# Optimization experiments

Measured on AMD Instinct MI355X. Metric: run time of the kernel, lower is better.

## Reference

```python
import jax, jax.numpy as jnp
import numpy as np
from jax import lax

D_MODEL = 512
INPUT_DIM = 64
D_INNER = 1024      # expand * d_model
D_STATE = 128
NHEADS = 16         # d_inner // headdim (headdim = ssm_state//num_heads = 64)
HEADDIM = 64
D_CONV = 4
CONV_DIM = D_INNER + 2 * D_STATE          # 1280 (ngroups=1)
D_IN_PROJ = 2 * D_INNER + 2 * D_STATE + NHEADS  # 2320
BATCH = 2
SEQ = 1024
MASK_RATIO = 0.75
EPS = 1e-5


def setup_inputs() -> dict:
    key = jax.random.key(0)
    ks = jax.random.split(key, 14)
    s = lambda fan: 1.0 / np.sqrt(fan)
    return {
        "x": jax.random.normal(ks[0], (BATCH, SEQ, INPUT_DIM), jnp.float32),
        "conv_emb_w": jax.random.normal(ks[1], (D_MODEL, INPUT_DIM, 3), jnp.float32) * s(INPUT_DIM * 3),
        "conv_emb_b": jax.random.normal(ks[2], (D_MODEL,), jnp.float32) * 0.02,
        "cls_token": jax.random.normal(ks[3], (1, 1, D_MODEL), jnp.float32) * 0.02,
        "in_proj_w": jax.random.normal(ks[4], (D_IN_PROJ, D_MODEL), jnp.float32) * s(D_MODEL),
        "conv1d_w": jax.random.normal(ks[5], (CONV_DIM, 1, D_CONV), jnp.float32) * s(D_CONV),
        "conv1d_b": jax.random.normal(ks[6], (CONV_DIM,), jnp.float32) * 0.02,
        "dt_bias": jax.random.uniform(ks[7], (NHEADS,), jnp.float32, -4.0, 0.0),
        "A_log": jnp.log(jax.random.uniform(ks[8], (NHEADS,), jnp.float32, 1.0, 16.0)),
        "D": jax.random.normal(ks[9], (NHEADS,), jnp.float32),
        "rms_w": jnp.ones((D_INNER,), jnp.float32),
        "out_proj_w": jax.random.normal(ks[10], (D_MODEL, D_INNER), jnp.float32) * s(D_INNER),
        "ln_g": jnp.ones((D_MODEL,), jnp.float32),
        "ln_b": jnp.zeros((D_MODEL,), jnp.float32),
    }


def _forward(x, conv_emb_w, conv_emb_b, cls_token, in_proj_w, conv1d_w, conv1d_b,
             dt_bias, A_log, D, rms_w, out_proj_w, ln_g, ln_b):
    b = x.shape[0]
    # ---- conv embedding: Conv1d(k=3, pad=1) over time ----
    xe = lax.conv_general_dilated(x.transpose(0, 2, 1), conv_emb_w, (1,), [(1, 1)],
                                  dimension_numbers=("NCH", "OIH", "NCH"))
    xe = (xe + conv_emb_b[None, :, None]).transpose(0, 2, 1)  # (b, L, d_model)
    # ---- append CLS token at end ----
    h = jnp.concatenate([xe, jnp.broadcast_to(cls_token, (b, 1, D_MODEL))], axis=1)
    L = h.shape[1]
    # ---- Mamba2 block ----
    zxbcdt = jnp.einsum("bld,ed->ble", h, in_proj_w)  # (b, L, 2320)
    z = zxbcdt[..., :D_INNER]
    xBC = zxbcdt[..., D_INNER:D_INNER + CONV_DIM]
    dt = jax.nn.softplus(zxbcdt[..., -NHEADS:] + dt_bias)  # (b, L, h)
    # causal depthwise conv (pad left d_conv-1) + SiLU
    xBC = lax.conv_general_dilated(xBC.transpose(0, 2, 1), conv1d_w, (1,), [(D_CONV - 1, 0)],
                                   dimension_numbers=("NCH", "OIH", "NCH"),
                                   feature_group_count=CONV_DIM)
    xBC = jax.nn.silu((xBC + conv1d_b[None, :, None]).transpose(0, 2, 1))  # (b, L, 1280)
    x_in = xBC[..., :D_INNER].reshape(b, L, NHEADS, HEADDIM)   # (b, L, h, p)
    B = xBC[..., D_INNER:D_INNER + D_STATE]                     # (b, L, n)
    C = xBC[..., D_INNER + D_STATE:]                            # (b, L, n)
    A = -jnp.exp(A_log)                                         # (h,)
    dA = jnp.exp(dt * A)                                        # (b, L, h)
    # selective state-space scan; state (b, h, p, n)
    def step(state, inp):
        x_t, dt_t, B_t, C_t, dA_t = inp  # (b,h,p) (b,h) (b,n) (b,n) (b,h)
        state = state * dA_t[:, :, None, None] + \
            (dt_t[:, :, None] * x_t)[..., None] * B_t[:, None, None, :]
        y_t = jnp.einsum("bhpn,bn->bhp", state, C_t)
        return state, y_t
    s0 = jnp.zeros((b, NHEADS, HEADDIM, D_STATE), x.dtype)
    _, ys = lax.scan(step, s0, (x_in.transpose(1, 0, 2, 3), dt.transpose(1, 0, 2),
                                B.transpose(1, 0, 2), C.transpose(1, 0, 2),
                                dA.transpose(1, 0, 2)))
    y = ys.transpose(1, 0, 2, 3) + D[None, None, :, None] * x_in  # (b, L, h, p)
    y = y.reshape(b, L, D_INNER)
    # gated RMSNorm: gate first, then normalize
    y = y * jax.nn.silu(z)
    y = y * lax.rsqrt(jnp.mean(y * y, axis=-1, keepdims=True) + EPS) * rms_w
    out = jnp.einsum("ble,de->bld", y, out_proj_w)  # (b, L, d_model)
    # ---- LayerNorm ----
    mu = jnp.mean(out, axis=-1, keepdims=True)
    var = jnp.mean((out - mu) ** 2, axis=-1, keepdims=True)
    out = (out - mu) * lax.rsqrt(var + EPS) * ln_g + ln_b
    return out


def reference(x, conv_emb_w, conv_emb_b, cls_token, in_proj_w, conv1d_w, conv1d_b,
              dt_bias, A_log, D, rms_w, out_proj_w, ln_g, ln_b):
    out = _forward(x, conv_emb_w, conv_emb_b, cls_token, in_proj_w, conv1d_w, conv1d_b,
                   dt_bias, A_log, D, rms_w, out_proj_w, ln_g, ln_b)
    b = out.shape[0]
    cls = out[:, -1:, :]
    body = out[:, :-1, :]                      # (b, SEQ, d)
    len_keep = int(SEQ * (1 - MASK_RATIO))     # 256
    noise = jax.random.uniform(jax.random.fold_in(jax.random.key(0), 1), (b, SEQ))
    ids_shuffle = jnp.argsort(noise, axis=1)
    ids_restore = jnp.argsort(ids_shuffle, axis=1)
    ids_keep = ids_shuffle[:, :len_keep]
    x_masked = jnp.take_along_axis(body, ids_keep[:, :, None], axis=1)
    mask = jnp.where(jnp.arange(SEQ)[None, :] < len_keep, 0.0, 1.0)
    mask = jnp.take_along_axis(jnp.broadcast_to(mask, (b, SEQ)), ids_restore, axis=1)
    x_out = jnp.concatenate([x_masked, cls], axis=1)  # (b, len_keep+1, d)
    return (x_out, mask, ids_restore, ids_keep)
```

## Files before the change

### kernel.cpp

```cpp
#include <hip/hip_runtime.h>
#include <hip/hip_bf16.h>
#include <stdint.h>

#define LTOK  1025
#define NROWS 2050
#define DM    512
#define DIN   1024
#define DST   128
#define NHEAD 16
#define HDIM  64
#define CDIM  1280
#define EPROJ 2320
#define QC    64
#define NCH   17

#define O_RIDX   0
#define O_CB     1024
#define O_CLS    1536
#define O_C1B    2048
#define O_DTB    3328
#define O_ALOG   3344
#define O_DV     3360
#define O_RMSW   3376
#define O_LNG    4400
#define O_LNB    4912
#define O_CW     5440
#define O_IPW    103744
#define O_OPW    1291584
#define O_C1W    1815872
#define O_CX     1820992
#define O_ZX     1952064
#define O_XBC    6708064
#define O_DT     9332064
#define O_LGA    9364864
#define O_Y      9397664
#define O_X3     10447264
#define O_OUTG   11496864
#define O_SL     11760032
#define O_CLA    16216480
#define O_SL2    16251296
#define O_KEEP   18479520
#define O_OUTP   18480128
#define O_CWT    19532800
#define O_W2     19581952
#define O_BIAS2  19804672

#define OO_MASK 263168
#define OO_IDR  265216
#define OO_IDK  267264

typedef __attribute__((ext_vector_type(8))) short short8;
typedef __attribute__((ext_vector_type(8))) unsigned short ushortx8;
typedef __attribute__((ext_vector_type(4))) float floatx4;

__device__ __forceinline__ short f2bs(float f) {
  union { float f; uint32_t u; } v; v.f = f;
  uint32_t r = (v.u + 0x7FFFu + ((v.u >> 16) & 1u)) >> 16;
  return (short)r;
}
__device__ __forceinline__ float bf2f(uint16_t u) {
  return __uint_as_float(((uint32_t)u) << 16);
}

struct InPtrs { const void* p[14]; };

__device__ __forceinline__ uint32_t rotl32(uint32_t v, int d) {
  return (v << d) | (v >> (32 - d));
}
__device__ void threefry2x32(uint32_t k0, uint32_t k1, uint32_t c0, uint32_t c1,
                             uint32_t& o0, uint32_t& o1) {
  uint32_t ks0 = k0, ks1 = k1, ks2 = 0x1BD11BDAu ^ k0 ^ k1;
  uint32_t x0 = c0 + ks0, x1 = c1 + ks1;
#define TF_R4(a,b,c,d) \
  x0 += x1; x1 = rotl32(x1,a); x1 ^= x0; \
  x0 += x1; x1 = rotl32(x1,b); x1 ^= x0; \
  x0 += x1; x1 = rotl32(x1,c); x1 ^= x0; \
  x0 += x1; x1 = rotl32(x1,d); x1 ^= x0;
  TF_R4(13,15,26,6)  x0 += ks1; x1 += ks2 + 1u;
  TF_R4(17,29,16,24) x0 += ks2; x1 += ks0 + 2u;
  TF_R4(13,15,26,6)  x0 += ks0; x1 += ks1 + 3u;
  TF_R4(17,29,16,24) x0 += ks1; x1 += ks2 + 4u;
  TF_R4(13,15,26,6)  x0 += ks2; x1 += ks0 + 5u;
#undef TF_R4
  o0 = x0; o1 = x1;
}

__device__ int detect_is_f32(const uint32_t* w, int nelem) {
  int nw = nelem / 2; if (nw > 16) nw = 16;
  int insane = 0, lozero = 0, anynz = 0;
  for (int i = 0; i < nw; ++i) {
    uint32_t word = w[i];
    if (word != 0u) anynz = 1;
    uint32_t lo = word & 0xffffu;
    if (lo == 0u) { lozero++; continue; }
    float v = __uint_as_float(lo << 16);
    float a = fabsf(v);
    if (!(a >= 1e-8f && a <= 1e4f)) insane++;
  }
  if (insane >= 2) return 1;
  if (lozero == nw && anynz) return 1;
  return 0;
}

__global__ __launch_bounds__(256) void k_convert(InPtrs ptrs, float* ws,
                                                 float* out, int* rowidx) {
  static const int sizes[13] = {98304, 512, 512, 1187840, 5120, 1280,
                                16, 16, 16, 1024, 524288, 512, 512};
  static const int offs[13]  = {O_CW, O_CB, O_CLS, O_IPW, O_C1W, O_C1B,
                                O_DTB, O_ALOG, O_DV, O_RMSW, O_OPW, O_LNG, O_LNB};
  static const int isbf[13]  = {1,0,0,1,0,0,0,0,0,0,1,0,0};
  static const int smallT[15] = {1,2,4,4,4,4,4,5,5,6,7,8,9,11,12};
  static const int smallB[15] = {0,0,0,1,2,3,4,0,1,0,0,0,0,0,0};
  int bx = blockIdx.x;
  int tid = threadIdx.x;

  if (bx < 2048) {
    int b = bx >> 10, idx = bx & 1023;
    const uint32_t* xp = (const uint32_t*)ptrs.p[0];
    __shared__ int xf;
    if (tid == 0) xf = detect_is_f32(xp, 131072);
    __syncthreads();
    if (tid < 192) {
      int i = tid / 3, k = tid % 3;
      int tt = idx + k - 1;
      float v = 0.f;
      if (tt >= 0 && tt < 1024) {
        long src = ((long)(b * 1024 + tt)) * 64 + i;
        v = xf ? ((const float*)xp)[src] : bf2f(((const uint16_t*)xp)[src]);
      }
      ((uint16_t*)(ws + O_X3))[((long)(b * 1024 + idx)) * 192 + tid] = (uint16_t)f2bs(v);
    }
    return;
  }
  bx -= 2048;

  int t, blk;
  if (bx < 1160) { t = 3; blk = bx; }
  else {
    bx -= 1160;
    if (bx < 512) { t = 10; blk = bx; }
    else {
      bx -= 512;
      if (bx < 96) {
        const uint32_t* w = (const uint32_t*)ptrs.p[1];
        __shared__ int sf;
        if (tid == 0) sf = detect_is_f32(w, 98304);
        __syncthreads();
        int base = (bx * 256 + tid) * 4;
        if (base >= 98304) return;
        uint16_t vv[4];
        if (sf) {
          const float4 f = *(const float4*)((const float*)w + base);
          vv[0] = (uint16_t)f2bs(f.x); vv[1] = (uint16_t)f2bs(f.y);
          vv[2] = (uint16_t)f2bs(f.z); vv[3] = (uint16_t)f2bs(f.w);
        } else {
          const uint32_t* s = w + (base >> 1);
          uint32_t w0 = s[0], w1 = s[1];
          vv[0] = (uint16_t)(w0 & 0xffffu); vv[1] = (uint16_t)(w0 >> 16);
          vv[2] = (uint16_t)(w1 & 0xffffu); vv[3] = (uint16_t)(w1 >> 16);
        }
        int o = base / 192, ik = base % 192;
        uint16_t* cwt = (uint16_t*)(ws + O_CWT);
#pragma unroll
        for (int j = 0; j < 4; ++j)
          cwt[(long)(ik + j) * 512 + o] = vv[j];
        return;
      }
      bx -= 96;
      if (bx < 32) {
        int seg = bx & 15, b = bx >> 4;
        uint8_t* keep = (uint8_t*)(ws + O_KEEP);
        __shared__ float vals[1024];
        uint32_t fk0, fk1;
        threefry2x32(0u, 0u, 0u, 1u, fk0, fk1);
#pragma unroll
        for (int k = 0; k < 4; ++k) {
          int i = tid + k * 256;
          uint32_t o0, o1;
          threefry2x32(fk0, fk1, 0u, (uint32_t)(b * 1024 + i), o0, o1);
          uint32_t bits = o0 ^ o1;
          vals[i] = __uint_as_float((bits >> 9) | 0x3f800000u) - 1.0f;
        }
        __syncthreads();
        int tg = seg * 64 + (tid >> 2);
        int qq = tid & 3;
        float v = vals[tg];
        int r = 0;
        int j0 = qq * 256;
        for (int it = 0; it < 256; ++it) {
          int j = j0 + ((it + qq * 8) & 255);
          float vj = vals[j];
          r += (vj < v || (vj == v && j < tg)) ? 1 : 0;
        }
        r += __shfl_xor(r, 1, 64);
        r += __shfl_xor(r, 2, 64);
        if (qq == 0) {
          out[OO_IDR + b * 1024 + tg] = (float)r;
          out[OO_MASK + b * 1024 + tg] = (r < 256) ? 0.0f : 1.0f;
          keep[b * LTOK + tg] = (r < 256) ? 1 : 0;
          if (r < 256) {
            out[OO_IDK + b * 256 + r] = (float)tg;
            rowidx[b * 257 + r] = b * LTOK + tg;
          }
          if (tg == 0) {
            rowidx[b * 257 + 256] = b * LTOK + 1024;
            keep[b * LTOK + 1024] = 1;
          }
        }
        return;
      }
      bx -= 32;
      if (bx >= 15) return;
      t = smallT[bx]; blk = smallB[bx];
    }
  }

  int n = sizes[t];
  const uint32_t* w = (const uint32_t*)ptrs.p[t + 1];
  __shared__ int sf;
  if (tid == 0) sf = detect_is_f32(w, n);
  __syncthreads();
  int base = (blk * 256 + tid) * 4;
  if (base >= n) return;
  if (isbf[t]) {
    ushort4 o;
    if (sf) {
      const float4 vv = *(const float4*)((const float*)w + base);
      o.x = (uint16_t)f2bs(vv.x); o.y = (uint16_t)f2bs(vv.y);
      o.z = (uint16_t)f2bs(vv.z); o.w = (uint16_t)f2bs(vv.w);
    } else {
      const uint32_t* s = w + (base >> 1);
      uint32_t w0 = s[0], w1 = s[1];
      o.x = (uint16_t)(w0 & 0xffffu); o.y = (uint16_t)(w0 >> 16);
      o.z = (uint16_t)(w1 & 0xffffu); o.w = (uint16_t)(w1 >> 16);
    }
    *(ushort4*)((uint16_t*)(ws + offs[t]) + base) = o;
  } else {
    float* dst = ws + offs[t];
    if (sf) {
      *(float4*)(dst + base) = *(const float4*)((const float*)w + base);
    } else {
      const uint32_t* s = w + (base >> 1);
      uint32_t w0 = s[0], w1 = s[1];
      float4 o;
      o.x = __uint_as_float((w0 & 0xffffu) << 16);
      o.y = __uint_as_float(w0 & 0xffff0000u);
      o.z = __uint_as_float((w1 & 0xffffu) << 16);
      o.w = __uint_as_float(w1 & 0xffff0000u);
      *(float4*)(dst + base) = o;
    }
  }
}

__global__ __launch_bounds__(256) void k_w2(const uint16_t* __restrict__ IPW,
                                            const uint16_t* __restrict__ CWT,
                                            const float* __restrict__ cb,
                                            const float* __restrict__ cls,
                                            uint16_t* __restrict__ W2,
                                            float* __restrict__ bias2,
                                            uint16_t* __restrict__ ZX) {
  int bx = blockIdx.x;
  int tid = threadIdx.x;

  if (bx >= 111) {
    __shared__ float scb[512];
    __shared__ float scl[512];
    for (int i = tid; i < 512; i += 256) {
      scb[i] = cb[i];
      scl[i] = bf2f((uint16_t)f2bs(cls[i]));
    }
    __syncthreads();
    int e = (bx - 111) * 232 + tid;
    if (tid < 232 && e < 2320) {
      float sb = 0.f, sc = 0.f;
      for (int d8 = 0; d8 < 512; d8 += 8) {
        ushortx8 v = *(const ushortx8*)(IPW + (long)e * 512 + d8);
#pragma unroll
        for (int j = 0; j < 8; ++j) {
          float wv = bf2f(v[j]);
          sb = fmaf(wv, scb[d8 + j], sb);
          sc = fmaf(wv, scl[d8 + j], sc);
        }
      }
      bias2[e] = sb;
      uint16_t cz = (uint16_t)f2bs(sc);
      ZX[(long)1024 * EPROJ + e] = cz;
      ZX[(long)2049 * EPROJ + e] = cz;
    }
    return;
  }

  int bm = bx / 3, bn = bx % 3;
  __shared__ __align__(16) short sA[64 * 136];
  __shared__ __align__(16) short sB[64 * 136];
  int lane = tid & 63, w = tid >> 6, lm = lane & 15, q = lane >> 4;

  floatx4 acc[4] = {};
  for (int ph = 0; ph < 4; ++ph) {
    int d0 = ph * 128;
#pragma unroll
    for (int it = 0; it < 4; ++it) {
      int li = it * 256 + tid;
      int row = li >> 4, col = (li & 15) * 8;
      int ge = bm * 64 + row;
      ushortx8 av = {0,0,0,0,0,0,0,0};
      if (ge < 2320) av = *(const ushortx8*)(IPW + (long)ge * 512 + d0 + col);
      *(ushortx8*)&sA[row * 136 + col] = av;
      ushortx8 bv = *(const ushortx8*)(CWT + (long)(bn * 64 + row) * 512 + d0 + col);
      *(ushortx8*)&sB[row * 136 + col] = bv;
    }
    __syncthreads();
#pragma unroll
    for (int kk = 0; kk < 4; ++kk) {
      short8 a = *(const short8*)&sA[(w * 16 + lm) * 136 + kk * 32 + q * 8];
#pragma unroll
      for (int ct = 0; ct < 4; ++ct) {
        short8 b = *(const short8*)&sB[(ct * 16 + lm) * 136 + kk * 32 + q * 8];
        acc[ct] = __builtin_amdgcn_mfma_f32_16x16x32_bf16(a, b, acc[ct], 0, 0, 0);
      }
    }
    __syncthreads();
  }
#pragma unroll
  for (int reg = 0; reg < 4; ++reg) {
    int e = bm * 64 + w * 16 + q * 4 + reg;
    if (e < 2320) {
#pragma unroll
      for (int ct = 0; ct < 4; ++ct)
        W2[(long)e * 192 + bn * 64 + ct * 16 + lm] = (uint16_t)f2bs(acc[ct][reg]);
    }
  }
}

__global__ __launch_bounds__(256) void k_ipgemm(const uint16_t* __restrict__ X3,
                                                const uint16_t* __restrict__ W2,
                                                const float* __restrict__ bias2,
                                                const uint8_t* __restrict__ keep,
                                                uint16_t* __restrict__ ZX) {
  __shared__ __align__(16) short sA[64 * 200];
  __shared__ __align__(16) short sB[64 * 200];
  __shared__ uint8_t skp[64];
  int tid = threadIdx.x;
  int lane = tid & 63, w = tid >> 6, lm = lane & 15, q = lane >> 4;
  int bm = blockIdx.y * 64, bn = blockIdx.x * 64;

  if (tid < 64) {
    int rr = bm + tid;
    skp[tid] = keep[(rr >> 10) * LTOK + (rr & 1023)];
  }
#pragma unroll
  for (int it = 0; it < 6; ++it) {
    int li = it * 256 + tid;
    int row = li / 24, col = (li % 24) * 8;
    ushortx8 av = *(const ushortx8*)(X3 + (long)(bm + row) * 192 + col);
    *(ushortx8*)&sA[row * 200 + col] = av;
    int gn = bn + row;
    ushortx8 bv = {0,0,0,0,0,0,0,0};
    if (gn < 2320) bv = *(const ushortx8*)(W2 + (long)gn * 192 + col);
    *(ushortx8*)&sB[row * 200 + col] = bv;
  }
  __syncthreads();

  floatx4 acc[4] = {};
#pragma unroll
  for (int kb = 0; kb < 6; ++kb) {
    short8 a = *(const short8*)&sA[(w * 16 + lm) * 200 + kb * 32 + q * 8];
#pragma unroll
    for (int ct = 0; ct < 4; ++ct) {
      short8 b = *(const short8*)&sB[(ct * 16 + lm) * 200 + kb * 32 + q * 8];
      acc[ct] = __builtin_amdgcn_mfma_f32_16x16x32_bf16(a, b, acc[ct], 0, 0, 0);
    }
  }
#pragma unroll
  for (int reg = 0; reg < 4; ++reg) {
    int r = bm + w * 16 + q * 4 + reg;
    long crow = (long)((r >> 10) * LTOK + (r & 1023));
    int kp = skp[r - bm];
#pragma unroll
    for (int ct = 0; ct < 4; ++ct) {
      int e = bn + ct * 16 + lm;
      if (e < 2320 && (e >= DIN || kp))
        ZX[crow * EPROJ + e] = (uint16_t)f2bs(acc[ct][reg] + bias2[e]);
    }
  }
}

__global__ __launch_bounds__(256) void k_conv1d(const uint16_t* __restrict__ zx,
                                                const float* __restrict__ w,
                                                const float* __restrict__ bias,
                                                uint16_t* __restrict__ xbc,
                                                const float* __restrict__ dtb,
                                                const float* __restrict__ alog,
                                                float* __restrict__ dt,
                                                float* __restrict__ lga) {
  int g = blockIdx.x;
  int tid = threadIdx.x;
  if (g >= 514) {
    int idx = (g - 514) * 256 + tid;
    if (idx < NROWS * NHEAD) {
      int rr = idx >> 4, h = idx & 15;
      float xv = bf2f(zx[(long)rr * EPROJ + (EPROJ - NHEAD) + h]) + dtb[h];
      float dtv = (xv > 20.f) ? xv : log1pf(expf(xv));
      dt[idx] = dtv;
      lga[idx] = dtv * (-expf(alog[h]));
    }
    return;
  }
  {
    int xcd = g & 7, slot = g >> 3;
    g = (xcd < 2) ? xcd * 65 + slot : 130 + (xcd - 2) * 64 + slot;
  }
  int b = g / 257, gi = g % 257;
  int t0 = gi * 4;
  int nr = (t0 == 1024) ? 1 : 4;
  const uint16_t* zrow = zx + (long)b * LTOK * EPROJ + DIN;
  for (int c4 = tid * 4; c4 < CDIM; c4 += 1024) {
    float4 bi = *(const float4*)(bias + c4);
    float4 w0 = *(const float4*)(w + (c4 + 0) * 4);
    float4 w1 = *(const float4*)(w + (c4 + 1) * 4);
    float4 w2 = *(const float4*)(w + (c4 + 2) * 4);
    float4 w3 = *(const float4*)(w + (c4 + 3) * 4);
    float wr[4][4] = {{w0.x, w0.y, w0.z, w0.w}, {w1.x, w1.y, w1.z, w1.w},
                      {w2.x, w2.y, w2.z, w2.w}, {w3.x, w3.y, w3.z, w3.w}};
    float acc[4][4];
#pragma unroll
    for (int ri = 0; ri < 4; ++ri) {
      acc[ri][0] = bi.x; acc[ri][1] = bi.y; acc[ri][2] = bi.z; acc[ri][3] = bi.w;
    }
#pragma unroll
    for (int dtt = -3; dtt <= 3; ++dtt) {
      int tt = t0 + dtt;
      if (tt < 0 || tt > 1024) continue;
      ushort4 xv = *(const ushort4*)(zrow + (long)tt * EPROJ + c4);
      float x0 = bf2f(xv.x), x1 = bf2f(xv.y), x2 = bf2f(xv.z), x3 = bf2f(xv.w);
#pragma unroll
      for (int ri = 0; ri < 4; ++ri) {
        int k = dtt - ri + 3;
        if (k >= 0 && k <= 3) {
          acc[ri][0] = fmaf(wr[0][k], x0, acc[ri][0]);
          acc[ri][1] = fmaf(wr[1][k], x1, acc[ri][1]);
          acc[ri][2] = fmaf(wr[2][k], x2, acc[ri][2]);
          acc[ri][3] = fmaf(wr[3][k], x3, acc[ri][3]);
        }
      }
    }
#pragma unroll
    for (int ri = 0; ri < 4; ++ri) {
      if (ri < nr) {
        long r = (long)b * LTOK + t0 + ri;
        ushort4 o;
        o.x = (uint16_t)f2bs(acc[ri][0] / (1.f + expf(-acc[ri][0])));
        o.y = (uint16_t)f2bs(acc[ri][1] / (1.f + expf(-acc[ri][1])));
        o.z = (uint16_t)f2bs(acc[ri][2] / (1.f + expf(-acc[ri][2])));
        o.w = (uint16_t)f2bs(acc[ri][3] / (1.f + expf(-acc[ri][3])));
        *(ushort4*)(xbc + r * CDIM + c4) = o;
      }
    }
  }
}

__global__ __launch_bounds__(256) void k_ssd1(const uint16_t* __restrict__ xbc,
                                              const float* __restrict__ dt,
                                              const float* __restrict__ lga,
                                              float* __restrict__ SL,
                                              float* __restrict__ CLA) {
  int blk = blockIdx.x;
  int c = blk % NCH;
  int hh = blk / NCH;
  int h = hh & 15, b = hh >> 4;
  int tid = threadIdx.x;
  int lane = tid & 63, w = tid >> 6;
  int lm = lane & 15, q = lane >> 4;

  __shared__ __align__(16) short sBT[128 * 72];
  __shared__ __align__(16) short sXT[64 * 72];
  __shared__ float wwv[64];

  int t0 = c * QC;
  const uint16_t* base = xbc + (long)b * LTOK * CDIM;

  if (tid < 64) {
    int t = t0 + tid;
    float dtv = (t < LTOK) ? dt[((long)(b * LTOK + t)) * NHEAD + h] : 0.f;
    float v   = (t < LTOK) ? lga[((long)(b * LTOK + t)) * NHEAD + h] : 0.f;
#pragma unroll
    for (int off = 1; off < 64; off <<= 1) {
      float u = __shfl_up(v, off, 64);
      if (lane >= off) v += u;
    }
    float clEnd = __shfl(v, 63, 64);
    wwv[tid] = __expf(clEnd - v) * dtv;
    CLA[(long)blk * 64 + tid] = v;
  }
  __syncthreads();

#pragma unroll
  for (int k = 0; k < 8; ++k) {
    int e4 = (tid + k * 256) * 4;
    int row = e4 >> 7, col = e4 & 127;
    int t = t0 + row;
    ushort4 bv = {0,0,0,0};
    if (t < LTOK) bv = *(const ushort4*)(base + (long)t * CDIM + DIN + col);
    float wv = wwv[row];
    sBT[(col  )*72+row]=f2bs(bf2f(bv.x)*wv); sBT[(col+1)*72+row]=f2bs(bf2f(bv.y)*wv);
    sBT[(col+2)*72+row]=f2bs(bf2f(bv.z)*wv); sBT[(col+3)*72+row]=f2bs(bf2f(bv.w)*wv);
  }
#pragma unroll
  for (int k = 0; k < 4; ++k) {
    int e4 = (tid + k * 256) * 4;
    int row = e4 >> 6, col = e4 & 63;
    int t = t0 + row;
    ushort4 xv = {0,0,0,0};
    if (t < LTOK) xv = *(const ushort4*)(base + (long)t * CDIM + h * 64 + col);
    sXT[(col  )*72+row]=(short)xv.x; sXT[(col+1)*72+row]=(short)xv.y;
    sXT[(col+2)*72+row]=(short)xv.z; sXT[(col+3)*72+row]=(short)xv.w;
  }
  __syncthreads();

  floatx4 s[2][4] = {};
#pragma unroll
  for (int kb = 0; kb < 2; ++kb) {
    short8 bfr[4];
#pragma unroll
    for (int ct = 0; ct < 4; ++ct)
      bfr[ct] = *(const short8*)&sXT[(ct*16 + lm)*72 + kb*32 + q*8];
#pragma unroll
    for (int nt = 0; nt < 2; ++nt) {
      short8 a = *(const short8*)&sBT[((w*2+nt)*16 + lm)*72 + kb*32 + q*8];
#pragma unroll
      for (int ct = 0; ct < 4; ++ct)
        s[nt][ct] = __builtin_amdgcn_mfma_f32_16x16x32_bf16(a, bfr[ct], s[nt][ct], 0, 0, 0);
    }
  }
  float* slp = SL + (long)blk * 8192;
#pragma unroll
  for (int nt = 0; nt < 2; ++nt)
#pragma unroll
    for (int ct = 0; ct < 4; ++ct)
#pragma unroll
      for (int reg = 0; reg < 4; ++reg) {
        int n = (w*2+nt)*16 + q*4 + reg;
        int p = ct*16 + lm;
        slp[n*64 + p] = s[nt][ct][reg];
      }
}

__global__ __launch_bounds__(256) void k_comb(const float* __restrict__ SL,
                                              const float* __restrict__ CLA,
                                              uint16_t* __restrict__ SL2) {
  int bx = blockIdx.x;
  int piece = bx & 15;
  int hh = bx >> 4;
  int off = piece * 512 + threadIdx.x * 2;
  long cb0 = (long)hh * NCH;
  float P[NCH];
  float2 tmp[NCH];
#pragma unroll
  for (int c = 0; c < NCH; ++c) {
    P[c] = __expf(CLA[(cb0 + c) * 64 + 63]);
    tmp[c] = *(const float2*)(SL + (cb0 + c) * 8192 + off);
  }
  float2 s = make_float2(0.f, 0.f);
#pragma unroll
  for (int c = 0; c < NCH; ++c) {
    uint32_t packed = (uint32_t)(uint16_t)f2bs(s.x) | ((uint32_t)(uint16_t)f2bs(s.y) << 16);
    *(uint32_t*)(SL2 + (cb0 + c) * 8192 + off) = packed;
    s.x = fmaf(P[c], s.x, tmp[c].x);
    s.y = fmaf(P[c], s.y, tmp[c].y);
  }
}

__global__ __launch_bounds__(256) void k_ssd3(const uint16_t* __restrict__ xbc,
                                              const float* __restrict__ dt,
                                              const uint16_t* __restrict__ SL2,
                                              const float* __restrict__ CLA,
                                              const uint8_t* __restrict__ keepf,
                                              float* __restrict__ Y) {
  int blk = blockIdx.x;
  int c = blk % NCH;
  int hh = blk / NCH;
  int h = hh & 15, b = hh >> 4;
  int tid = threadIdx.x;
  int lane = tid & 63, w = tid >> 6;
  int lm = lane & 15, q = lane >> 4;

  __shared__ __align__(16) short sST[64 * 136];
  __shared__ __align__(16) short sXT[64 * 72];
  __shared__ __align__(16) short sM[64 * 72];
  __shared__ float dtw[64], clA[64], evec[64];
  __shared__ uint8_t kf[64];

  int t0 = c * QC;
  const uint16_t* base = xbc + (long)b * LTOK * CDIM;
  const uint16_t* slp = SL2 + (long)blk * 8192;

  if (tid < 64) {
    int t = t0 + tid;
    dtw[tid] = (t < LTOK) ? dt[((long)(b * LTOK + t)) * NHEAD + h] : 0.f;
    float v = CLA[(long)blk * 64 + tid];
    clA[tid] = v;
    evec[tid] = __expf(v);
    kf[tid] = (t < LTOK) ? keepf[b * LTOK + t] : 0;
  }

#pragma unroll
  for (int k = 0; k < 4; ++k) {
    int e4 = (tid + k * 256) * 4;
    int row = e4 >> 6, col = e4 & 63;
    int t = t0 + row;
    ushort4 xv = {0,0,0,0};
    if (t < LTOK) xv = *(const ushort4*)(base + (long)t * CDIM + h * 64 + col);
    sXT[(col  )*72+row]=(short)xv.x; sXT[(col+1)*72+row]=(short)xv.y;
    sXT[(col+2)*72+row]=(short)xv.z; sXT[(col+3)*72+row]=(short)xv.w;
  }
#pragma unroll
  for (int k = 0; k < 8; ++k) {
    int e4 = (tid + k * 256) * 4;
    int n = e4 >> 6, p = e4 & 63;
    ushort4 sv = *(const ushort4*)(slp + n * 64 + p);
    sST[(p  )*136+n]=(short)sv.x; sST[(p+1)*136+n]=(short)sv.y;
    sST[(p+2)*136+n]=(short)sv.z; sST[(p+3)*136+n]=(short)sv.w;
  }
  __syncthreads();

  short8 cfr[4];
  int tA = t0 + w*16 + lm;
  bool tAok = tA < LTOK;
#pragma unroll
  for (int kb = 0; kb < 4; ++kb) {
    short8 z = {0,0,0,0,0,0,0,0};
    cfr[kb] = tAok ? *(const short8*)(base + (long)tA * CDIM + DIN + DST + kb*32 + q*8) : z;
  }

  floatx4 g[4] = {};
#pragma unroll
  for (int kb = 0; kb < 4; ++kb) {
#pragma unroll
    for (int ct = 0; ct < 4; ++ct) {
      int tB = t0 + ct*16 + lm;
      short8 z = {0,0,0,0,0,0,0,0};
      short8 bb = (tB < LTOK) ? *(const short8*)(base + (long)tB * CDIM + DIN + kb*32 + q*8) : z;
      g[ct] = __builtin_amdgcn_mfma_f32_16x16x32_bf16(cfr[kb], bb, g[ct], 0, 0, 0);
    }
  }
#pragma unroll
  for (int ct = 0; ct < 4; ++ct) {
    int tp = ct*16 + lm;
#pragma unroll
    for (int reg = 0; reg < 4; ++reg) {
      int tl = w*16 + q*4 + reg;
      float m = 0.f;
      if (tp <= tl) m = g[ct][reg] * __expf(clA[tl] - clA[tp]) * dtw[tp];
      sM[tl*72 + tp] = f2bs(m);
    }
  }
  floatx4 y2[4] = {};
#pragma unroll
  for (int kb = 0; kb < 4; ++kb) {
#pragma unroll
    for (int ct = 0; ct < 4; ++ct) {
      short8 bb = *(const short8*)&sST[(ct*16 + lm)*136 + kb*32 + q*8];
      y2[ct] = __builtin_amdgcn_mfma_f32_16x16x32_bf16(cfr[kb], bb, y2[ct], 0, 0, 0);
    }
  }
  __syncthreads();
  floatx4 y1[4] = {};
#pragma unroll
  for (int kb = 0; kb < 2; ++kb) {
    short8 a = *(const short8*)&sM[(w*16 + lm)*72 + kb*32 + q*8];
#pragma unroll
    for (int ct = 0; ct < 4; ++ct) {
      short8 bb = *(const short8*)&sXT[(ct*16 + lm)*72 + kb*32 + q*8];
      y1[ct] = __builtin_amdgcn_mfma_f32_16x16x32_bf16(a, bb, y1[ct], 0, 0, 0);
    }
  }
#pragma unroll
  for (int reg = 0; reg < 4; ++reg) {
    int tl = w*16 + q*4 + reg;
    int t = t0 + tl;
    if (t < LTOK && kf[tl]) {
      float ev = evec[tl];
#pragma unroll
      for (int ct = 0; ct < 4; ++ct) {
        int p = ct*16 + lm;
        Y[((long)(b * LTOK + t)) * DIN + h * 64 + p] = y1[ct][reg] + ev * y2[ct][reg];
      }
    }
  }
}

__global__ __launch_bounds__(256) void k_gaterms(const float* __restrict__ Y,
                                                 const uint16_t* __restrict__ xbc,
                                                 const uint16_t* __restrict__ zx,
                                                 const float* __restrict__ Dv,
                                                 const float* __restrict__ rmsw,
                                                 const int* __restrict__ ridx,
                                                 uint16_t* __restrict__ G) {
  int rr = blockIdx.x;
  long r = ridx[rr];
  int tid = threadIdx.x;
  int e = tid * 4;
  int h = tid >> 4;
  float4 a = *(const float4*)(Y + r * DIN + e);
  const ushort4 xu = *(const ushort4*)(xbc + r * CDIM + e);
  const ushort4 zu = *(const ushort4*)(zx + r * EPROJ + e);
  float Dh = Dv[h];
  float y0 = a.x + Dh * bf2f(xu.x), y1 = a.y + Dh * bf2f(xu.y);
  float y2 = a.z + Dh * bf2f(xu.z), y3 = a.w + Dh * bf2f(xu.w);
  float z0 = bf2f(zu.x), z1 = bf2f(zu.y), z2 = bf2f(zu.z), z3 = bf2f(zu.w);
  float g0 = y0 * (z0 / (1.f + expf(-z0)));
  float g1 = y1 * (z1 / (1.f + expf(-z1)));
  float g2 = y2 * (z2 / (1.f + expf(-z2)));
  float g3 = y3 * (z3 / (1.f + expf(-z3)));
  __shared__ float red[256];
  red[tid] = g0*g0 + g1*g1 + g2*g2 + g3*g3;
  __syncthreads();
  for (int st = 128; st; st >>= 1) {
    if (tid < st) red[tid] += red[tid + st];
    __syncthreads();
  }
  float scale = rsqrtf(red[0] * (1.0f / 1024.0f) + 1e-5f);
  float4 rw = *(const float4*)(rmsw + e);
  ushort4 o;
  o.x = (uint16_t)f2bs(g0 * scale * rw.x);
  o.y = (uint16_t)f2bs(g1 * scale * rw.y);
  o.z = (uint16_t)f2bs(g2 * scale * rw.z);
  o.w = (uint16_t)f2bs(g3 * scale * rw.w);
  *(ushort4*)(G + (long)rr * DIN + e) = o;
}

__global__ __launch_bounds__(256) void k_ogemm(const uint16_t* __restrict__ A,
                                               const uint16_t* __restrict__ Bw,
                                               float* __restrict__ OUTP) {
  __shared__ __align__(16) short sA[64 * 264];
  __shared__ __align__(16) short sB[64 * 264];
  int tid = threadIdx.x;
  int lane = tid & 63, w = tid >> 6;
  int lm = lane & 15, q = lane >> 4;
  int bm = blockIdx.y * 64, bn = blockIdx.x * 64;
  int kbase = blockIdx.z * 256;

#pragma unroll
  for (int it = 0; it < 8; ++it) {
    int li = it * 256 + tid;
    int row = li >> 5, col = (li & 31) * 8;
    int gm = bm + row;
    ushortx8 av = {0,0,0,0,0,0,0,0};
    if (gm < 514) av = *(const ushortx8*)(A + (long)gm * 1024 + kbase + col);
    *(ushortx8*)&sA[row * 264 + col] = av;
    ushortx8 bv = *(const ushortx8*)(Bw + (long)(bn + row) * 1024 + kbase + col);
    *(ushortx8*)&sB[row * 264 + col] = bv;
  }
  __syncthreads();

  floatx4 acc[4] = {};
#pragma unroll
  for (int kb = 0; kb < 8; ++kb) {
    short8 a = *(const short8*)&sA[(w * 16 + lm) * 264 + kb * 32 + q * 8];
#pragma unroll
    for (int ct = 0; ct < 4; ++ct) {
      short8 b = *(const short8*)&sB[(ct * 16 + lm) * 264 + kb * 32 + q * 8];
      acc[ct] = __builtin_amdgcn_mfma_f32_16x16x32_bf16(a, b, acc[ct], 0, 0, 0);
    }
  }
  float* op = OUTP + (long)blockIdx.z * 263168;
#pragma unroll
  for (int reg = 0; reg < 4; ++reg) {
    int r = bm + w * 16 + q * 4 + reg;
    if (r < 514) {
#pragma unroll
      for (int ct = 0; ct < 4; ++ct)
        op[(long)r * 512 + bn + ct * 16 + lm] = acc[ct][reg];
    }
  }
}

__global__ __launch_bounds__(256) void k_ln(const float* __restrict__ outp,
                                            const float* __restrict__ lng,
                                            const float* __restrict__ lnb,
                                            float* __restrict__ out) {
  int r = blockIdx.x;
  int tid = threadIdx.x;
  long e = (long)r * DM + tid * 2;
  float2 v0 = *(const float2*)(outp + e);
  float2 v1 = *(const float2*)(outp + 263168 + e);
  float2 v2 = *(const float2*)(outp + 2 * 263168 + e);
  float2 v3 = *(const float2*)(outp + 3 * 263168 + e);
  float2 v;
  v.x = ((v0.x + v1.x) + v2.x) + v3.x;
  v.y = ((v0.y + v1.y) + v2.y) + v3.y;
  __shared__ float red[256];
  red[tid] = v.x + v.y;
  __syncthreads();
  for (int st = 128; st; st >>= 1) { if (tid < st) red[tid] += red[tid + st]; __syncthreads(); }
  float mu = red[0] * (1.0f / 512.0f);
  __syncthreads();
  float dx = v.x - mu, dy = v.y - mu;
  red[tid] = dx * dx + dy * dy;
  __syncthreads();
  for (int st = 128; st; st >>= 1) { if (tid < st) red[tid] += red[tid + st]; __syncthreads(); }
  float sc = rsqrtf(red[0] * (1.0f / 512.0f) + 1e-5f);
  int c = tid * 2;
  out[(long)r * DM + c]     = dx * sc * lng[c] + lnb[c];
  out[(long)r * DM + c + 1] = dy * sc * lng[c + 1] + lnb[c + 1];
}

extern "C" void kernel_launch(void* const* d_in, const int* in_sizes, int n_in,
                              void* d_out, int out_size, void* d_ws, size_t ws_size,
                              hipStream_t stream) {
  float* ws = (float*)d_ws;
  float* out = (float*)d_out;
  int* rowidx = (int*)(ws + O_RIDX);
  InPtrs ip;
  for (int i = 0; i < 14; ++i) ip.p[i] = d_in[i];

  hipLaunchKernelGGL(k_convert, dim3(3863), dim3(256), 0, stream, ip, ws, out, rowidx);
  hipLaunchKernelGGL(k_w2, dim3(121), dim3(256), 0, stream,
                     (const uint16_t*)(ws + O_IPW), (const uint16_t*)(ws + O_CWT),
                     ws + O_CB, ws + O_CLS,
                     (uint16_t*)(ws + O_W2), ws + O_BIAS2, (uint16_t*)(ws + O_ZX));
  hipLaunchKernelGGL(k_ipgemm, dim3(37, 32), dim3(256), 0, stream,
                     (const uint16_t*)(ws + O_X3), (const uint16_t*)(ws + O_W2),
                     ws + O_BIAS2, (const uint8_t*)(ws + O_KEEP),
                     (uint16_t*)(ws + O_ZX));
  hipLaunchKernelGGL(k_conv1d, dim3(643), dim3(256), 0, stream,
                     (const uint16_t*)(ws + O_ZX), ws + O_C1W, ws + O_C1B,
                     (uint16_t*)(ws + O_XBC),
                     ws + O_DTB, ws + O_ALOG, ws + O_DT, ws + O_LGA);
  hipLaunchKernelGGL(k_ssd1, dim3(32 * NCH), dim3(256), 0, stream,
                     (const uint16_t*)(ws + O_XBC), ws + O_DT, ws + O_LGA,
                     ws + O_SL, ws + O_CLA);
  hipLaunchKernelGGL(k_comb, dim3(512), dim3(256), 0, stream,
                     ws + O_SL, ws + O_CLA, (uint16_t*)(ws + O_SL2));
  hipLaunchKernelGGL(k_ssd3, dim3(32 * NCH), dim3(256), 0, stream,
                     (const uint16_t*)(ws + O_XBC), ws + O_DT,
                     (const uint16_t*)(ws + O_SL2), ws + O_CLA,
                     (const uint8_t*)(ws + O_KEEP), ws + O_Y);
  hipLaunchKernelGGL(k_gaterms, dim3(514), dim3(256), 0, stream,
                     ws + O_Y, (const uint16_t*)(ws + O_XBC),
                     (const uint16_t*)(ws + O_ZX), ws + O_DV, ws + O_RMSW,
                     (const int*)rowidx, (uint16_t*)(ws + O_X3));
  hipLaunchKernelGGL(k_ogemm, dim3(8, 9, 4), dim3(256), 0, stream,
                     (const uint16_t*)(ws + O_X3), (const uint16_t*)(ws + O_OPW),
                     ws + O_OUTP);
  hipLaunchKernelGGL(k_ln, dim3(514), dim3(256), 0, stream,
                     ws + O_OUTP, ws + O_LNG, ws + O_LNB, out);
}
```

Measured before the change: 186.9 us.

## Vectorize im2col conversion with k-major layout and double k-tile in W2 GEMM

The input-to-im2col conversion now handles 8 rows per block with 8-wide vector loads and stores. The tap-major ordering (k*64+i) replaces the interleaved one, and the conv weight transpose is permuted to match. This cuts the conversion grid from 2048 blocks to 256 and removes scalar per-element traffic. The W2 precompute GEMM also loads 256-wide K tiles in two phases instead of four, which halves the barriers but uses more LDS per block.

```diff
diff --git a/kernel.cpp b/kernel.cpp
--- a/kernel.cpp
+++ b/kernel.cpp
@@ -114,25 +114,37 @@
   int bx = blockIdx.x;
   int tid = threadIdx.x;
 
-  if (bx < 2048) {
-    int b = bx >> 10, idx = bx & 1023;
+  if (bx < 256) {
     const uint32_t* xp = (const uint32_t*)ptrs.p[0];
     __shared__ int xf;
     if (tid == 0) xf = detect_is_f32(xp, 131072);
     __syncthreads();
     if (tid < 192) {
-      int i = tid / 3, k = tid % 3;
-      int tt = idx + k - 1;
-      float v = 0.f;
+      int r = bx * 8 + tid / 24;
+      int seg = tid % 24;
+      int kk = seg >> 3, i0 = (seg & 7) * 8;
+      int b = r >> 10, idx = r & 1023;
+      int tt = idx + kk - 1;
+      ushortx8 o = {0,0,0,0,0,0,0,0};
       if (tt >= 0 && tt < 1024) {
-        long src = ((long)(b * 1024 + tt)) * 64 + i;
-        v = xf ? ((const float*)xp)[src] : bf2f(((const uint16_t*)xp)[src]);
+        long src = ((long)(b * 1024 + tt)) * 64 + i0;
+        if (xf) {
+          const float* xfp = (const float*)xp;
+          float4 f0 = *(const float4*)(xfp + src);
+          float4 f1 = *(const float4*)(xfp + src + 4);
+          o[0] = (uint16_t)f2bs(f0.x); o[1] = (uint16_t)f2bs(f0.y);
+          o[2] = (uint16_t)f2bs(f0.z); o[3] = (uint16_t)f2bs(f0.w);
+          o[4] = (uint16_t)f2bs(f1.x); o[5] = (uint16_t)f2bs(f1.y);
+          o[6] = (uint16_t)f2bs(f1.z); o[7] = (uint16_t)f2bs(f1.w);
+        } else {
+          o = *(const ushortx8*)((const uint16_t*)xp + src);
+        }
       }
-      ((uint16_t*)(ws + O_X3))[((long)(b * 1024 + idx)) * 192 + tid] = (uint16_t)f2bs(v);
+      *(ushortx8*)((uint16_t*)(ws + O_X3) + (long)r * 192 + kk * 64 + i0) = o;
     }
     return;
   }
-  bx -= 2048;
+  bx -= 256;
 
   int t, blk;
   if (bx < 1160) { t = 3; blk = bx; }
@@ -162,8 +174,11 @@
         int o = base / 192, ik = base % 192;
         uint16_t* cwt = (uint16_t*)(ws + O_CWT);
 #pragma unroll
-        for (int j = 0; j < 4; ++j)
-          cwt[(long)(ik + j) * 512 + o] = vv[j];
+        for (int j = 0; j < 4; ++j) {
+          int ikj = ik + j;
+          int kp = (ikj % 3) * 64 + (ikj / 3);
+          cwt[(long)kp * 512 + o] = vv[j];
+        }
         return;
       }
       bx -= 96;
@@ -291,31 +306,31 @@
   }
 
   int bm = bx / 3, bn = bx % 3;
-  __shared__ __align__(16) short sA[64 * 136];
-  __shared__ __align__(16) short sB[64 * 136];
+  __shared__ __align__(16) short sA[64 * 264];
+  __shared__ __align__(16) short sB[64 * 264];
   int lane = tid & 63, w = tid >> 6, lm = lane & 15, q = lane >> 4;
 
   floatx4 acc[4] = {};
-  for (int ph = 0; ph < 4; ++ph) {
-    int d0 = ph * 128;
-#pragma unroll
-    for (int it = 0; it < 4; ++it) {
+  for (int ph = 0; ph < 2; ++ph) {
+    int d0 = ph * 256;
+#pragma unroll
+    for (int it = 0; it < 8; ++it) {
       int li = it * 256 + tid;
-      int row = li >> 4, col = (li & 15) * 8;
+      int row = li >> 5, col = (li & 31) * 8;
       int ge = bm * 64 + row;
       ushortx8 av = {0,0,0,0,0,0,0,0};
       if (ge < 2320) av = *(const ushortx8*)(IPW + (long)ge * 512 + d0 + col);
-      *(ushortx8*)&sA[row * 136 + col] = av;
+      *(ushortx8*)&sA[row * 264 + col] = av;
       ushortx8 bv = *(const ushortx8*)(CWT + (long)(bn * 64 + row) * 512 + d0 + col);
-      *(ushortx8*)&sB[row * 136 + col] = bv;
+      *(ushortx8*)&sB[row * 264 + col] = bv;
     }
     __syncthreads();
 #pragma unroll
-    for (int kk = 0; kk < 4; ++kk) {
-      short8 a = *(const short8*)&sA[(w * 16 + lm) * 136 + kk * 32 + q * 8];
+    for (int kk = 0; kk < 8; ++kk) {
+      short8 a = *(const short8*)&sA[(w * 16 + lm) * 264 + kk * 32 + q * 8];
 #pragma unroll
       for (int ct = 0; ct < 4; ++ct) {
-        short8 b = *(const short8*)&sB[(ct * 16 + lm) * 136 + kk * 32 + q * 8];
+        short8 b = *(const short8*)&sB[(ct * 16 + lm) * 264 + kk * 32 + q * 8];
         acc[ct] = __builtin_amdgcn_mfma_f32_16x16x32_bf16(a, b, acc[ct], 0, 0, 0);
       }
     }
@@ -814,7 +829,7 @@
   InPtrs ip;
   for (int i = 0; i < 14; ++i) ip.p[i] = d_in[i];
 
-  hipLaunchKernelGGL(k_convert, dim3(3863), dim3(256), 0, stream, ip, ws, out, rowidx);
+  hipLaunchKernelGGL(k_convert, dim3(2071), dim3(256), 0, stream, ip, ws, out, rowidx);
   hipLaunchKernelGGL(k_w2, dim3(121), dim3(256), 0, stream,
                      (const uint16_t*)(ws + O_IPW), (const uint16_t*)(ws + O_CWT),
                      ws + O_CB, ws + O_CLS,
```

Result: no change. 183.8 us (-1.7%).
